# Kernel optimization log

Hardware: AMD Instinct MI355X
Metric: run time of the kernel (lower is better)

Reference implementation:

```python
import jax, jax.numpy as jnp
import numpy as np

NUM_EMB = 1024
EMB_DIM = 256
COMMITMENT_COST = 0.25


def setup_inputs() -> dict:
    key = jax.random.key(0)
    k1, k2 = jax.random.split(key)
    inp = jax.random.normal(k1, (64, EMB_DIM, 32, 32), dtype=jnp.float32)  # [B, C, H, W]
    emb_weight = jax.random.uniform(
        k2, (NUM_EMB, EMB_DIM), minval=-1.0 / NUM_EMB, maxval=1.0 / NUM_EMB, dtype=jnp.float32
    )
    return {"inp": inp, "emb_weight": emb_weight}


def reference(inp, emb_weight):
    sg = jax.lax.stop_gradient
    x = jnp.transpose(inp, (0, 2, 3, 1))              # [B, H, W, C]
    flat = x.reshape(-1, EMB_DIM)                      # [N, C]
    d = (jnp.sum(flat * flat, axis=1, keepdims=True)
         + jnp.sum(emb_weight * emb_weight, axis=1)
         - 2.0 * (flat @ emb_weight.T))
    idx = jnp.argmin(d, axis=1)                        # [N]
    encodings = jax.nn.one_hot(idx, NUM_EMB, dtype=jnp.float32)  # [N, K]
    e = emb_weight[idx].reshape(x.shape)               # [B, H, W, C]
    loss = jnp.mean((e - sg(x)) ** 2) + COMMITMENT_COST * jnp.mean((sg(e) - x) ** 2)
    e_ste = x + sg(e - x)                              # straight-through estimator
    avg_probs = jnp.mean(encodings, axis=0)
    perplexity = jnp.exp(-jnp.sum(avg_probs * jnp.log(avg_probs + 1e-10)))
    out = jnp.transpose(e_ste, (0, 3, 1, 2))           # back to [B, C, H, W]
    return loss, out, perplexity, encodings
```

## Files before the change

kernel.cpp:

```cpp
#include <hip/hip_runtime.h>
#include <hip/hip_bf16.h>
#include <math.h>
#include <float.h>

#define BB    64
#define CCH   256
#define KKE   1024
#define HWN   1024
#define NTOT  (BB*HWN)
#define OUT_ELE (BB*CCH*HWN)
#define LOSS_OFF 0
#define OUT_OFF  1
#define PERP_OFF (1 + OUT_ELE)
#define ENC_OFF  (2 + OUT_ELE)

#define WS_IDX    0
#define WS_ANORM  262144
#define WS_HIST   524288
#define WS_BNORM  528384
#define WS_MISC   532480
#define WS_LIST   536576
#define WS_EMBT   798720
#define WS_EHI    1847296
#define WS_ELO    2371584
#define WS_CD1    2895872
#define WS_CK1    4993024
#define WS_CD2    7090176
#define WS_AHI    9187328
#define WS_ALO    42741760

typedef __attribute__((ext_vector_type(4))) float f32x4;
typedef __attribute__((ext_vector_type(8))) short s16x8;

#define TAU 2e-4f

__device__ __forceinline__ void gload16(const short* g, void* l) {
    __builtin_amdgcn_global_load_lds(
        (const __attribute__((address_space(1))) unsigned int*)g,
        (__attribute__((address_space(3))) unsigned int*)l,
        16, 0, 0);
}

__device__ inline void merge_cand(float& d1, int& k1, float& d2,
                                  float od1, int ok1, float od2) {
    bool w = (od1 < d1) || (od1 == d1 && ok1 < k1);
    float loser_d1 = w ? d1 : od1;
    float winner_d2 = w ? od2 : d2;
    d2 = fminf(winner_d2, loser_d1);
    if (w) { d1 = od1; k1 = ok1; }
}

__global__ __launch_bounds__(256) void prep_kernel(const float* __restrict__ emb,
                                                   float* __restrict__ embT,
                                                   float* __restrict__ bnorm,
                                                   short* __restrict__ ehi,
                                                   short* __restrict__ elo,
                                                   unsigned int* __restrict__ hist,
                                                   float* __restrict__ misc) {
    const int k = blockIdx.x;
    const int t = threadIdx.x;
    float v = emb[k*CCH + t];
    embT[(size_t)t*KKE + k] = v;
    __hip_bfloat16 h = __float2bfloat16(v);
    float hf = __bfloat162float(h);
    __hip_bfloat16 l = __float2bfloat16(v - hf);
    const int u  = (t & 31) >> 3;
    const int sw = (k >> 1) & 3;
    size_t eoff = (size_t)(t >> 5)*32768 + (size_t)k*32 + (size_t)((u ^ sw)*8 + (t & 7));
    ehi[eoff] = *(short*)&h;
    elo[eoff] = *(short*)&l;
    double sq = (double)v * (double)v;
    #pragma unroll
    for (int off = 32; off; off >>= 1) sq += __shfl_down(sq, off);
    __shared__ double wred[4];
    const int wave = t >> 6, lane = t & 63;
    if (lane == 0) wred[wave] = sq;
    __syncthreads();
    if (t == 0) bnorm[k] = (float)(wred[0] + wred[1] + wred[2] + wred[3]);
    if (blockIdx.x < 4) hist[blockIdx.x*256 + t] = 0u;
    if (blockIdx.x == 4 && t == 0) { misc[0] = 0.0f; ((int*)misc)[1] = 0; }
}

__global__ __launch_bounds__(256) void asplit_kernel(const float* __restrict__ inp,
                                                     short* __restrict__ ahi,
                                                     short* __restrict__ alo,
                                                     float* __restrict__ anorm) {
    const int t  = threadIdx.x;
    const int b  = blockIdx.y;
    const int hw = blockIdx.x * 256 + t;
    const int n  = b * HWN + hw;
    const float* src = inp + (size_t)b*CCH*HWN + hw;
    const int sw = (n >> 1) & 3;
    double s = 0.0;
    for (int chunk = 0; chunk < 8; ++chunk) {
        s16x8 hs[4], ls[4];
        #pragma unroll
        for (int cc = 0; cc < 32; ++cc) {
            float v = src[(size_t)(chunk*32 + cc)*HWN];
            s += (double)v * (double)v;
            __hip_bfloat16 h = __float2bfloat16(v);
            float hf = __bfloat162float(h);
            __hip_bfloat16 l = __float2bfloat16(v - hf);
            hs[cc >> 3][cc & 7] = *(short*)&h;
            ls[cc >> 3][cc & 7] = *(short*)&l;
        }
        const size_t obase = ((size_t)chunk*NTOT + (size_t)n) * 32;
        #pragma unroll
        for (int u = 0; u < 4; ++u) {
            *(s16x8*)&ahi[obase + (size_t)((u ^ sw) * 8)] = hs[u];
            *(s16x8*)&alo[obase + (size_t)((u ^ sw) * 8)] = ls[u];
        }
    }
    anorm[n] = (float)s;
}

__global__ __launch_bounds__(256, 3) void argmin_mfma(const short* __restrict__ ahi,
                                                      const short* __restrict__ alo,
                                                      const short* __restrict__ ehi,
                                                      const short* __restrict__ elo,
                                                      const float* __restrict__ anorm,
                                                      const float* __restrict__ bnorm,
                                                      float* __restrict__ cd1,
                                                      int* __restrict__ ck1,
                                                      float* __restrict__ cd2) {
    __shared__ short smem[4][4096];

    const int t    = threadIdx.x;
    const int w    = t >> 6;
    const int lane = t & 63;
    const int q    = lane >> 4;
    const int l15  = lane & 15;
    const int n0   = blockIdx.x * 128;
    const int k0   = blockIdx.y * 128;

    f32x4 acc[2][8];
    #pragma unroll
    for (int i = 0; i < 2; ++i)
        #pragma unroll
        for (int j = 0; j < 8; ++j) acc[i][j] = (f32x4){0.f,0.f,0.f,0.f};

    const int swu = (q ^ ((l15 >> 1) & 3)) << 4;
    const int ra0 = (w*32 + l15)*64 + swu;

    for (int chunk = 0; chunk < 8; ++chunk) {
        __syncthreads();
        {
            const short* as = ahi + (size_t)chunk*2097152 + (size_t)n0*32;
            const short* al = alo + (size_t)chunk*2097152 + (size_t)n0*32;
            const short* bs = ehi + (size_t)chunk*32768  + (size_t)k0*32;
            const short* bl = elo + (size_t)chunk*32768  + (size_t)k0*32;
            #pragma unroll
            for (int i = 0; i < 2; ++i) {
                const size_t so = (size_t)i*2048 + (size_t)t*8;
                const int    lo = i*4096 + w*1024;
                gload16(as + so, (char*)&smem[0][0] + lo);
                gload16(al + so, (char*)&smem[1][0] + lo);
                gload16(bs + so, (char*)&smem[2][0] + lo);
                gload16(bl + so, (char*)&smem[3][0] + lo);
            }
        }
        __syncthreads();
        const char* LAh = (const char*)&smem[0][0];
        const char* LAl = (const char*)&smem[1][0];
        const char* LBh = (const char*)&smem[2][0];
        const char* LBl = (const char*)&smem[3][0];
        s16x8 afh0 = *(const s16x8*)(LAh + ra0);
        s16x8 afh1 = *(const s16x8*)(LAh + ra0 + 1024);
        s16x8 afl0 = *(const s16x8*)(LAl + ra0);
        s16x8 afl1 = *(const s16x8*)(LAl + ra0 + 1024);
        #pragma unroll
        for (int ct = 0; ct < 8; ++ct) {
            const int rb = (ct*16 + l15)*64 + swu;
            s16x8 bh = *(const s16x8*)(LBh + rb);
            s16x8 bl = *(const s16x8*)(LBl + rb);
            acc[0][ct] = __builtin_amdgcn_mfma_f32_16x16x32_bf16(afh0, bh, acc[0][ct], 0, 0, 0);
            acc[0][ct] = __builtin_amdgcn_mfma_f32_16x16x32_bf16(afh0, bl, acc[0][ct], 0, 0, 0);
            acc[0][ct] = __builtin_amdgcn_mfma_f32_16x16x32_bf16(afl0, bh, acc[0][ct], 0, 0, 0);
            acc[1][ct] = __builtin_amdgcn_mfma_f32_16x16x32_bf16(afh1, bh, acc[1][ct], 0, 0, 0);
            acc[1][ct] = __builtin_amdgcn_mfma_f32_16x16x32_bf16(afh1, bl, acc[1][ct], 0, 0, 0);
            acc[1][ct] = __builtin_amdgcn_mfma_f32_16x16x32_bf16(afl1, bh, acc[1][ct], 0, 0, 0);
        }
    }

    float bnv[8];
    #pragma unroll
    for (int ct = 0; ct < 8; ++ct) bnv[ct] = bnorm[k0 + ct*16 + l15];

    #pragma unroll
    for (int rg = 0; rg < 2; ++rg) {
        #pragma unroll
        for (int reg = 0; reg < 4; ++reg) {
            const int n = n0 + w*32 + rg*16 + q*4 + reg;
            const float a = anorm[n];
            float d1 = FLT_MAX, d2 = FLT_MAX; int k1 = 0;
            #pragma unroll
            for (int ct = 0; ct < 8; ++ct) {
                float s = a + bnv[ct];
                float d = s - 2.0f * acc[rg][ct][reg];
                int   k = k0 + ct*16 + l15;
                if (d < d1 || (d == d1 && k < k1)) { d2 = d1; d1 = d; k1 = k; }
                else d2 = fminf(d2, d);
            }
            #pragma unroll
            for (int off = 1; off < 16; off <<= 1) {
                float od1 = __shfl_xor(d1, off);
                int   ok1 = __shfl_xor(k1, off);
                float od2 = __shfl_xor(d2, off);
                merge_cand(d1, k1, d2, od1, ok1, od2);
            }
            if (l15 == 0) {
                const size_t o = (size_t)blockIdx.y*NTOT + n;
                cd1[o] = d1; ck1[o] = k1; cd2[o] = d2;
            }
        }
    }
}

__global__ __launch_bounds__(256) void reduce_kernel(const float* __restrict__ cd1,
                                                     const int* __restrict__ ck1,
                                                     const float* __restrict__ cd2,
                                                     int* __restrict__ idx,
                                                     int* __restrict__ list,
                                                     int* __restrict__ counter) {
    const int n = blockIdx.x*256 + threadIdx.x;
    float d1 = cd1[n]; int k1 = ck1[n]; float d2 = cd2[n];
    #pragma unroll
    for (int kb = 1; kb < 8; ++kb) {
        const size_t o = (size_t)kb*NTOT + n;
        merge_cand(d1, k1, d2, cd1[o], ck1[o], cd2[o]);
    }
    idx[n] = k1;
    if (d2 - d1 < TAU) {
        int p = atomicAdd(counter, 1);
        list[p] = n;
    }
}

__global__ __launch_bounds__(256) void rescore_kernel(const float* __restrict__ inp,
                                                      const float* __restrict__ embT,
                                                      const float* __restrict__ anorm,
                                                      const float* __restrict__ bnorm,
                                                      const int* __restrict__ list,
                                                      const int* __restrict__ counter,
                                                      int* __restrict__ idx) {
    __shared__ float xs[256];
    __shared__ float rd[256];
    __shared__ int   rk[256];
    const int t = threadIdx.x;
    const int cnt = *counter;
    for (int f = blockIdx.x; f < cnt; f += gridDim.x) {
        const int n = list[f];
        const int b = n >> 10, hw = n & 1023;
        __syncthreads();
        xs[t] = inp[(size_t)b*CCH*HWN + (size_t)t*HWN + hw];
        __syncthreads();
        float dot0 = 0.f, dot1 = 0.f, dot2 = 0.f, dot3 = 0.f;
        #pragma unroll 4
        for (int c = 0; c < CCH; ++c) {
            const float xc = xs[c];
            const float* row = embT + (size_t)c*KKE + t;
            dot0 += xc * row[0];
            dot1 += xc * row[256];
            dot2 += xc * row[512];
            dot3 += xc * row[768];
        }
        const float a = anorm[n];
        float bd = FLT_MAX; int bk = 0;
        float dots[4] = {dot0, dot1, dot2, dot3};
        #pragma unroll
        for (int kk = 0; kk < 4; ++kk) {
            const int k = kk*256 + t;
            float s = a + bnorm[k];
            float d = s - 2.0f * dots[kk];
            if (d < bd || (d == bd && k < bk)) { bd = d; bk = k; }
        }
        rd[t] = bd; rk[t] = bk;
        __syncthreads();
        for (int stride = 128; stride; stride >>= 1) {
            if (t < stride) {
                float od = rd[t+stride]; int ok = rk[t+stride];
                if (od < rd[t] || (od == rd[t] && ok < rk[t])) { rd[t] = od; rk[t] = ok; }
            }
            __syncthreads();
        }
        if (t == 0) idx[n] = rk[0];
    }
}

__global__ __launch_bounds__(256) void onehot_kernel(const int* __restrict__ idx,
                                                     float* __restrict__ enc,
                                                     unsigned int* __restrict__ hist) {
    const int t = threadIdx.x;
    const int j4 = t * 4;
    for (int r = 0; r < 16; ++r) {
        const int n = blockIdx.x*16 + r;
        const int k = idx[n];
        float2 v0 = {0.0f, 0.0f}, v1 = {0.0f, 0.0f};
        if (k == j4)     v0.x = 1.0f;
        if (k == j4 + 1) v0.y = 1.0f;
        if (k == j4 + 2) v1.x = 1.0f;
        if (k == j4 + 3) v1.y = 1.0f;
        float* row = enc + (size_t)n * KKE;
        *(float2*)&row[j4]     = v0;
        *(float2*)&row[j4 + 2] = v1;
        if (t == 0) atomicAdd(&hist[k], 1u);
    }
}

__global__ __launch_bounds__(256) void out_loss_kernel(const float* __restrict__ inp,
                                                       const float* __restrict__ embT,
                                                       const int* __restrict__ idx,
                                                       float* __restrict__ out,
                                                       float* __restrict__ lossacc) {
    const int t = threadIdx.x;
    const size_t stride = (size_t)gridDim.x * 256;
    float lsum = 0.0f;
    for (size_t m = (size_t)blockIdx.x * 256 + t; m < (size_t)OUT_ELE; m += stride) {
        int hw = (int)(m & 1023);
        int c  = (int)((m >> 10) & 255);
        int b  = (int)(m >> 18);
        int k  = idx[b*HWN + hw];
        float e = embT[(size_t)c*KKE + k];
        float x = inp[m];
        out[m] = e;
        float df = e - x;
        lsum += df * df;
    }
    #pragma unroll
    for (int off = 32; off; off >>= 1) lsum += __shfl_down(lsum, off);
    __shared__ float wred[4];
    const int wave = t >> 6, lane = t & 63;
    if (lane == 0) wred[wave] = lsum;
    __syncthreads();
    if (t == 0) atomicAdd(lossacc, wred[0] + wred[1] + wred[2] + wred[3]);
}

__global__ __launch_bounds__(1024) void final_kernel(const unsigned int* __restrict__ hist,
                                                     const float* __restrict__ lossacc,
                                                     float* __restrict__ d_out) {
    const int t = threadIdx.x;
    float p = (float)hist[t] * (1.0f / 65536.0f);
    float v = p * logf(p + 1e-10f);
    #pragma unroll
    for (int off = 32; off; off >>= 1) v += __shfl_down(v, off);
    __shared__ float wred[16];
    const int wave = t >> 6, lane = t & 63;
    if (lane == 0) wred[wave] = v;
    __syncthreads();
    if (t == 0) {
        float s = 0.0f;
        #pragma unroll
        for (int i = 0; i < 16; ++i) s += wred[i];
        d_out[PERP_OFF] = expf(-s);
        d_out[LOSS_OFF] = 1.25f * (*lossacc) * (1.0f / (float)OUT_ELE);
    }
}

extern "C" void kernel_launch(void* const* d_in, const int* in_sizes, int n_in,
                              void* d_out, int out_size, void* d_ws, size_t ws_size,
                              hipStream_t stream) {
    (void)in_sizes; (void)n_in; (void)out_size; (void)ws_size;
    const float* inp = (const float*)d_in[0];
    const float* emb = (const float*)d_in[1];
    float* out = (float*)d_out;
    char* ws = (char*)d_ws;
    int*          idx     = (int*)(ws + WS_IDX);
    float*        anorm   = (float*)(ws + WS_ANORM);
    unsigned int* hist    = (unsigned int*)(ws + WS_HIST);
    float*        bnorm   = (float*)(ws + WS_BNORM);
    float*        misc    = (float*)(ws + WS_MISC);
    int*          list    = (int*)(ws + WS_LIST);
    float*        embT    = (float*)(ws + WS_EMBT);
    short*        ehi     = (short*)(ws + WS_EHI);
    short*        elo     = (short*)(ws + WS_ELO);
    float*        cd1     = (float*)(ws + WS_CD1);
    int*          ck1     = (int*)(ws + WS_CK1);
    float*        cd2     = (float*)(ws + WS_CD2);
    short*        ahi     = (short*)(ws + WS_AHI);
    short*        alo     = (short*)(ws + WS_ALO);
    int*          counter = ((int*)misc) + 1;

    prep_kernel<<<dim3(KKE), dim3(256), 0, stream>>>(emb, embT, bnorm, ehi, elo, hist, misc);
    asplit_kernel<<<dim3(4, BB), dim3(256), 0, stream>>>(inp, ahi, alo, anorm);
    argmin_mfma<<<dim3(512, 8), dim3(256), 0, stream>>>(ahi, alo, ehi, elo, anorm, bnorm, cd1, ck1, cd2);
    reduce_kernel<<<dim3(256), dim3(256), 0, stream>>>(cd1, ck1, cd2, idx, list, counter);
    rescore_kernel<<<dim3(512), dim3(256), 0, stream>>>(inp, embT, anorm, bnorm, list, counter, idx);
    onehot_kernel<<<dim3(4096), dim3(256), 0, stream>>>(idx, out + ENC_OFF, hist);
    out_loss_kernel<<<dim3(4096), dim3(256), 0, stream>>>(inp, embT, idx, out + OUT_OFF, misc);
    final_kernel<<<dim3(1), dim3(1024), 0, stream>>>(hist, misc, out);
}
```

Measured before the change: 742.3 us.

## Batch rescore over 8 rows and fuse one-hot with output/loss kernel

The rescore kernel now handles 8 listed rows per block iteration, so each embedding column load is reused across 8 dot products. The per-row tree reduction through shared memory is replaced by wave shuffles plus a small cross-wave pass. The one-hot and output/loss kernels are merged into one launch split by block index, and the one-hot stores are widened to float4. The enc offset (2 + OUT_ELE) is only 8-byte aligned, so the float4 stores are shifted by two floats with the row edges handled separately. The aims are less launch overhead and less global traffic in rescore, at the cost of more registers per thread.

```diff
diff --git a/kernel.cpp b/kernel.cpp
--- a/kernel.cpp
+++ b/kernel.cpp
@@ -33,6 +33,7 @@
 typedef __attribute__((ext_vector_type(8))) short s16x8;
 
 #define TAU 2e-4f
+#define RB  8
 
 __device__ __forceinline__ void gload16(const short* g, void* l) {
     __builtin_amdgcn_global_load_lds(
@@ -243,96 +244,143 @@
                                                       const int* __restrict__ list,
                                                       const int* __restrict__ counter,
                                                       int* __restrict__ idx) {
-    __shared__ float xs[256];
-    __shared__ float rd[256];
-    __shared__ int   rk[256];
+    __shared__ float xs[RB][256];
+    __shared__ float wd[RB][4];
+    __shared__ int   wk[RB][4];
+    __shared__ int   ls[RB];
     const int t = threadIdx.x;
+    const int wave = t >> 6, lane = t & 63;
     const int cnt = *counter;
-    for (int f = blockIdx.x; f < cnt; f += gridDim.x) {
-        const int n = list[f];
-        const int b = n >> 10, hw = n & 1023;
-        __syncthreads();
-        xs[t] = inp[(size_t)b*CCH*HWN + (size_t)t*HWN + hw];
-        __syncthreads();
-        float dot0 = 0.f, dot1 = 0.f, dot2 = 0.f, dot3 = 0.f;
+    const int ngrp = (cnt + RB - 1) / RB;
+    float bn[4];
+    #pragma unroll
+    for (int kk = 0; kk < 4; ++kk) bn[kk] = bnorm[kk*256 + t];
+
+    for (int g = blockIdx.x; g < ngrp; g += gridDim.x) {
+        const int base = g * RB;
+        const int m = min(RB, cnt - base);
+        __syncthreads();
+        if (t < RB) ls[t] = list[base + ((t < m) ? t : 0)];
+        __syncthreads();
+        #pragma unroll
+        for (int j = 0; j < RB; ++j) {
+            const int n = ls[j];
+            xs[j][t] = inp[(size_t)(n >> 10)*CCH*HWN + (size_t)t*HWN + (n & 1023)];
+        }
+        __syncthreads();
+        float dots[RB][4];
+        #pragma unroll
+        for (int j = 0; j < RB; ++j)
+            #pragma unroll
+            for (int kk = 0; kk < 4; ++kk) dots[j][kk] = 0.f;
         #pragma unroll 4
         for (int c = 0; c < CCH; ++c) {
-            const float xc = xs[c];
             const float* row = embT + (size_t)c*KKE + t;
-            dot0 += xc * row[0];
-            dot1 += xc * row[256];
-            dot2 += xc * row[512];
-            dot3 += xc * row[768];
-        }
-        const float a = anorm[n];
-        float bd = FLT_MAX; int bk = 0;
-        float dots[4] = {dot0, dot1, dot2, dot3};
-        #pragma unroll
-        for (int kk = 0; kk < 4; ++kk) {
-            const int k = kk*256 + t;
-            float s = a + bnorm[k];
-            float d = s - 2.0f * dots[kk];
-            if (d < bd || (d == bd && k < bk)) { bd = d; bk = k; }
-        }
-        rd[t] = bd; rk[t] = bk;
-        __syncthreads();
-        for (int stride = 128; stride; stride >>= 1) {
-            if (t < stride) {
-                float od = rd[t+stride]; int ok = rk[t+stride];
-                if (od < rd[t] || (od == rd[t] && ok < rk[t])) { rd[t] = od; rk[t] = ok; }
-            }
-            __syncthreads();
-        }
-        if (t == 0) idx[n] = rk[0];
-    }
-}
-
-__global__ __launch_bounds__(256) void onehot_kernel(const int* __restrict__ idx,
-                                                     float* __restrict__ enc,
-                                                     unsigned int* __restrict__ hist) {
+            const float e0 = row[0], e1 = row[256], e2 = row[512], e3 = row[768];
+            #pragma unroll
+            for (int j = 0; j < RB; ++j) {
+                const float xc = xs[j][c];
+                dots[j][0] += xc * e0;
+                dots[j][1] += xc * e1;
+                dots[j][2] += xc * e2;
+                dots[j][3] += xc * e3;
+            }
+        }
+        #pragma unroll
+        for (int j = 0; j < RB; ++j) {
+            const float a = anorm[ls[j]];
+            float bd = FLT_MAX; int bk = 0;
+            #pragma unroll
+            for (int kk = 0; kk < 4; ++kk) {
+                const int k = kk*256 + t;
+                float s = a + bn[kk];
+                float d = s - 2.0f * dots[j][kk];
+                if (d < bd || (d == bd && k < bk)) { bd = d; bk = k; }
+            }
+            #pragma unroll
+            for (int off = 1; off < 64; off <<= 1) {
+                float od = __shfl_xor(bd, off);
+                int   ok = __shfl_xor(bk, off);
+                if (od < bd || (od == bd && ok < bk)) { bd = od; bk = ok; }
+            }
+            if (lane == 0) { wd[j][wave] = bd; wk[j][wave] = bk; }
+        }
+        __syncthreads();
+        if (t < m) {
+            float bd = wd[t][0]; int bk = wk[t][0];
+            #pragma unroll
+            for (int wv = 1; wv < 4; ++wv) {
+                float od = wd[t][wv]; int ok = wk[t][wv];
+                if (od < bd || (od == bd && ok < bk)) { bd = od; bk = ok; }
+            }
+            idx[ls[t]] = bk;
+        }
+    }
+}
+
+#define ENC_BLK 2048
+#define OL_BLK  4096
+__global__ __launch_bounds__(256) void tail_kernel(const float* __restrict__ inp,
+                                                   const float* __restrict__ embT,
+                                                   const int* __restrict__ idx,
+                                                   float* __restrict__ enc,
+                                                   float* __restrict__ out,
+                                                   unsigned int* __restrict__ hist,
+                                                   float* __restrict__ lossacc) {
     const int t = threadIdx.x;
-    const int j4 = t * 4;
-    for (int r = 0; r < 16; ++r) {
-        const int n = blockIdx.x*16 + r;
-        const int k = idx[n];
-        float2 v0 = {0.0f, 0.0f}, v1 = {0.0f, 0.0f};
-        if (k == j4)     v0.x = 1.0f;
-        if (k == j4 + 1) v0.y = 1.0f;
-        if (k == j4 + 2) v1.x = 1.0f;
-        if (k == j4 + 3) v1.y = 1.0f;
-        float* row = enc + (size_t)n * KKE;
-        *(float2*)&row[j4]     = v0;
-        *(float2*)&row[j4 + 2] = v1;
-        if (t == 0) atomicAdd(&hist[k], 1u);
-    }
-}
-
-__global__ __launch_bounds__(256) void out_loss_kernel(const float* __restrict__ inp,
-                                                       const float* __restrict__ embT,
-                                                       const int* __restrict__ idx,
-                                                       float* __restrict__ out,
-                                                       float* __restrict__ lossacc) {
-    const int t = threadIdx.x;
-    const size_t stride = (size_t)gridDim.x * 256;
-    float lsum = 0.0f;
-    for (size_t m = (size_t)blockIdx.x * 256 + t; m < (size_t)OUT_ELE; m += stride) {
-        int hw = (int)(m & 1023);
-        int c  = (int)((m >> 10) & 255);
-        int b  = (int)(m >> 18);
-        int k  = idx[b*HWN + hw];
-        float e = embT[(size_t)c*KKE + k];
-        float x = inp[m];
-        out[m] = e;
-        float df = e - x;
-        lsum += df * df;
-    }
-    #pragma unroll
-    for (int off = 32; off; off >>= 1) lsum += __shfl_down(lsum, off);
-    __shared__ float wred[4];
-    const int wave = t >> 6, lane = t & 63;
-    if (lane == 0) wred[wave] = lsum;
-    __syncthreads();
-    if (t == 0) atomicAdd(lossacc, wred[0] + wred[1] + wred[2] + wred[3]);
+    if (blockIdx.x < ENC_BLK) {
+        const int n0 = blockIdx.x * 32;
+        int kr[32];
+        #pragma unroll
+        for (int r4 = 0; r4 < 8; ++r4) {
+            int4 kv = *(const int4*)&idx[n0 + r4*4];
+            kr[r4*4+0] = kv.x; kr[r4*4+1] = kv.y; kr[r4*4+2] = kv.z; kr[r4*4+3] = kv.w;
+        }
+        const int j4 = t*4 + 2;
+        #pragma unroll 8
+        for (int r = 0; r < 32; ++r) {
+            const int k = kr[r];
+            float* row = enc + (size_t)(n0 + r) * KKE;
+            if (t < 255) {
+                float4 v = {0.f,0.f,0.f,0.f};
+                if (k == j4)     v.x = 1.f;
+                if (k == j4 + 1) v.y = 1.f;
+                if (k == j4 + 2) v.z = 1.f;
+                if (k == j4 + 3) v.w = 1.f;
+                *(float4*)&row[j4] = v;
+            } else {
+                float2 h  = {0.f,0.f}, tl = {0.f,0.f};
+                if (k == 0)    h.x  = 1.f;
+                if (k == 1)    h.y  = 1.f;
+                if (k == 1022) tl.x = 1.f;
+                if (k == 1023) tl.y = 1.f;
+                *(float2*)&row[0]    = h;
+                *(float2*)&row[1022] = tl;
+            }
+            if (t == 0) atomicAdd(&hist[k], 1u);
+        }
+    } else {
+        const size_t stride = (size_t)OL_BLK * 256;
+        float lsum = 0.0f;
+        for (size_t m = (size_t)(blockIdx.x - ENC_BLK) * 256 + t; m < (size_t)OUT_ELE; m += stride) {
+            int hw = (int)(m & 1023);
+            int c  = (int)((m >> 10) & 255);
+            int b  = (int)(m >> 18);
+            int k  = idx[b*HWN + hw];
+            float e = embT[(size_t)c*KKE + k];
+            float x = inp[m];
+            out[m] = e;
+            float df = e - x;
+            lsum += df * df;
+        }
+        #pragma unroll
+        for (int off = 32; off; off >>= 1) lsum += __shfl_down(lsum, off);
+        __shared__ float wred[4];
+        const int wave = t >> 6, lane = t & 63;
+        if (lane == 0) wred[wave] = lsum;
+        __syncthreads();
+        if (t == 0) atomicAdd(lossacc, wred[0] + wred[1] + wred[2] + wred[3]);
+    }
 }
 
 __global__ __launch_bounds__(1024) void final_kernel(const unsigned int* __restrict__ hist,
@@ -385,7 +433,6 @@
     argmin_mfma<<<dim3(512, 8), dim3(256), 0, stream>>>(ahi, alo, ehi, elo, anorm, bnorm, cd1, ck1, cd2);
     reduce_kernel<<<dim3(256), dim3(256), 0, stream>>>(cd1, ck1, cd2, idx, list, counter);
     rescore_kernel<<<dim3(512), dim3(256), 0, stream>>>(inp, embT, anorm, bnorm, list, counter, idx);
-    onehot_kernel<<<dim3(4096), dim3(256), 0, stream>>>(idx, out + ENC_OFF, hist);
-    out_loss_kernel<<<dim3(4096), dim3(256), 0, stream>>>(inp, embT, idx, out + OUT_OFF, misc);
+    tail_kernel<<<dim3(ENC_BLK + OL_BLK), dim3(256), 0, stream>>>(inp, embT, idx, out + ENC_OFF, out + OUT_OFF, hist, misc);
     final_kernel<<<dim3(1), dim3(1024), 0, stream>>>(hist, misc, out);
 }
```

After: 653.5 us. 12.0% less time.
